# Kernel optimization log

Measured on AMD Instinct MI355X. Metric: run time of the kernel, lower is better.

## Reference

```python
import jax, jax.numpy as jnp
import numpy as np

CACHE_LEN = 1024
EPS = 1e-5

def layer_norm(x, g, b):
    m = jnp.mean(x, axis=-1, keepdims=True)
    var = jnp.mean(jnp.square(x - m), axis=-1, keepdims=True)
    return (x - m) * jax.lax.rsqrt(var + EPS) * g + b

def setup_inputs() -> dict:
    key = jax.random.key(0)
    ks = jax.random.split(key, 16)
    B, Lq, Lk, D_IN, D_OUT = 4, 4096, 5119, 512, 512
    s = 1.0 / np.sqrt(D_IN)
    return {
        "q": jax.random.normal(ks[0], (B, Lq, D_IN), jnp.float32),
        "k": jax.random.normal(ks[1], (B, Lk, D_IN), jnp.float32),
        "v": jax.random.normal(ks[2], (B, Lk, D_IN), jnp.float32),
        "gq": jnp.ones((D_IN,), jnp.float32),
        "bq": jnp.zeros((D_IN,), jnp.float32),
        "gk": jnp.ones((D_IN,), jnp.float32),
        "bk": jnp.zeros((D_IN,), jnp.float32),
        "gv": jnp.ones((D_IN,), jnp.float32),
        "bv": jnp.zeros((D_IN,), jnp.float32),
        "Wq": jax.random.uniform(ks[3], (D_IN, D_OUT), jnp.float32, -s, s),
        "bwq": jax.random.uniform(ks[4], (D_OUT,), jnp.float32, -s, s),
        "Wk": jax.random.uniform(ks[5], (D_IN, D_OUT), jnp.float32, -s, s),
        "bwk": jax.random.uniform(ks[6], (D_OUT,), jnp.float32, -s, s),
        "Wv": jax.random.uniform(ks[7], (D_IN, D_OUT), jnp.float32, -s, s),
        "bwv": jax.random.uniform(ks[8], (D_OUT,), jnp.float32, -s, s),
    }

def reference(q, k, v, gq, bq, gk, bk, gv, bv, Wq, bwq, Wk, bwk, Wv, bwv):
    B, Lq, _ = q.shape
    Lk = k.shape[1]
    qp = layer_norm(q, gq, bq) @ Wq + bwq            # [B,Lq,Do]
    kp = layer_norm(k, gk, bk) @ Wk + bwk            # [B,Lk,Do]
    vp = layer_norm(v, gv, bv) @ Wv + bwv            # [B,Lk,Do]
    kv = jax.nn.relu(kp) * vp                         # [B,Lk,Do]
    # integrate3 skew-pad builds a banded ones mask: query row i attends to
    # kv columns [sup+i, sup+i+cache_len-1]. Equivalent sliding-window sum
    # computed via prefix sums (O(Lk*d) instead of O(Lq*Lk*d)).
    sup = Lk - Lq - CACHE_LEN + 1
    cs = jnp.cumsum(kv, axis=1)
    cs = jnp.concatenate([jnp.zeros_like(cs[:, :1]), cs], axis=1)  # [B,Lk+1,Do]
    starts = sup + jnp.arange(Lq)
    weighted = cs[:, starts + CACHE_LEN] - cs[:, starts]            # [B,Lq,Do]
    return jax.nn.relu(qp) * weighted
```

## Files before the change

kernel.cpp:

```cpp
#include <hip/hip_runtime.h>

#define B     4
#define LQ    4096
#define LK    5119
#define D     512
#define CACHE 1024
#define MQ    (B * LQ)
#define MK    (B * LK)
#define MKP   20480
#define NCH   160
#define TI    32

typedef float  f32x4  __attribute__((ext_vector_type(4)));
typedef __bf16 bf16x2 __attribute__((ext_vector_type(2)));
typedef __bf16 bf16x4 __attribute__((ext_vector_type(4)));
typedef __bf16 bf16x8 __attribute__((ext_vector_type(8)));

__device__ __forceinline__ void async16(void* lds, const void* g)
{
    __builtin_amdgcn_global_load_lds(
        (__attribute__((address_space(1))) void*)(g),
        (__attribute__((address_space(3))) void*)(lds),
        16, 0, 0);
}

__global__ __launch_bounds__(64) void ln_kernel(
    const float* __restrict__ q, const float* __restrict__ k,
    const float* __restrict__ v,
    const float* __restrict__ gq, const float* __restrict__ bq,
    const float* __restrict__ gk, const float* __restrict__ bk,
    const float* __restrict__ gv, const float* __restrict__ bv,
    __bf16* __restrict__ qn, __bf16* __restrict__ kn, __bf16* __restrict__ vn)
{
    const int z = blockIdx.y;
    const float *x, *g, *bb; __bf16* o; int M;
    if (z == 0)      { x = q; g = gq; bb = bq; o = qn; M = MQ; }
    else if (z == 1) { x = k; g = gk; bb = bk; o = kn; M = MK; }
    else             { x = v; g = gv; bb = bv; o = vn; M = MK; }
    const int r = blockIdx.x;
    if (r >= M) return;

    const int t = threadIdx.x;
    const float* xr = x + (long)r * D;
    const float4 a0 = *reinterpret_cast<const float4*>(xr + t * 4);
    const float4 a1 = *reinterpret_cast<const float4*>(xr + 256 + t * 4);

    float s  = a0.x + a0.y + a0.z + a0.w + a1.x + a1.y + a1.z + a1.w;
    float ss = a0.x*a0.x + a0.y*a0.y + a0.z*a0.z + a0.w*a0.w
             + a1.x*a1.x + a1.y*a1.y + a1.z*a1.z + a1.w*a1.w;
#pragma unroll
    for (int m = 1; m < 64; m <<= 1) {
        s  += __shfl_xor(s,  m, 64);
        ss += __shfl_xor(ss, m, 64);
    }
    const float mean = s * (1.f / (float)D);
    const float var  = ss * (1.f / (float)D) - mean * mean;
    const float rs   = rsqrtf(var + 1e-5f);

    const float4 g0 = *reinterpret_cast<const float4*>(g + t * 4);
    const float4 g1 = *reinterpret_cast<const float4*>(g + 256 + t * 4);
    const float4 b0 = *reinterpret_cast<const float4*>(bb + t * 4);
    const float4 b1 = *reinterpret_cast<const float4*>(bb + 256 + t * 4);

    bf16x4 o0, o1;
    o0[0] = (__bf16)((a0.x - mean) * rs * g0.x + b0.x);
    o0[1] = (__bf16)((a0.y - mean) * rs * g0.y + b0.y);
    o0[2] = (__bf16)((a0.z - mean) * rs * g0.z + b0.z);
    o0[3] = (__bf16)((a0.w - mean) * rs * g0.w + b0.w);
    o1[0] = (__bf16)((a1.x - mean) * rs * g1.x + b1.x);
    o1[1] = (__bf16)((a1.y - mean) * rs * g1.y + b1.y);
    o1[2] = (__bf16)((a1.z - mean) * rs * g1.z + b1.z);
    o1[3] = (__bf16)((a1.w - mean) * rs * g1.w + b1.w);

    __bf16* orow = o + (long)r * D;
    *reinterpret_cast<bf16x4*>(orow + t * 4)       = o0;
    *reinterpret_cast<bf16x4*>(orow + 256 + t * 4) = o1;
}

__global__ __launch_bounds__(256) void wconv_kernel(
    const float* __restrict__ Wq, const float* __restrict__ Wk,
    const float* __restrict__ Wv,
    __bf16* __restrict__ wtq, __bf16* __restrict__ wtk, __bf16* __restrict__ wtv)
{
    const int z = blockIdx.z;
    const float* W = (z == 0) ? Wq : (z == 1) ? Wk : Wv;
    __bf16*     Wt = (z == 0) ? wtq : (z == 1) ? wtk : wtv;
    const int n  = blockIdx.x * 256 + threadIdx.x;
    const int k0 = blockIdx.y * 8;
    bf16x8 o;
#pragma unroll
    for (int j = 0; j < 8; ++j)
        o[j] = (__bf16)W[(long)(k0 + j) * D + n];
    *reinterpret_cast<bf16x8*>(Wt + (long)n * D + k0) = o;
}

__global__ __launch_bounds__(256) void gemm_q_kernel(
    const __bf16* __restrict__ A, const __bf16* __restrict__ Wt,
    const float* __restrict__ bias, __bf16* __restrict__ Cout)
{
    __shared__ __attribute__((aligned(16))) __bf16 As[128 * 32];
    __shared__ __attribute__((aligned(16))) __bf16 Bs[128 * 32];

    const int tid  = threadIdx.x;
    const int lane = tid & 63;
    const int wave = tid >> 6;
    const int quad = lane >> 4;
    const int l16  = lane & 15;
    const int wm   = wave >> 1;
    const int wn   = wave & 1;

    f32x4 acc[4][4];
#pragma unroll
    for (int i = 0; i < 4; ++i)
#pragma unroll
        for (int j = 0; j < 4; ++j)
            acc[i][j] = (f32x4){0.f, 0.f, 0.f, 0.f};

    const long arow0 = (long)blockIdx.x * 128;
    const long brow0 = (long)blockIdx.y * 128;
    const int  srow  = lane >> 2;
    const int  scol  = (lane & 3) * 8;

    for (int k0 = 0; k0 < D; k0 += 32) {
#pragma unroll
        for (int h = 0; h < 2; ++h) {
            const int chunk = h * 4 + wave;
            const int row   = chunk * 16 + srow;
            async16(&As[chunk * 512], &A [(arow0 + row) * D + k0 + scol]);
            async16(&Bs[chunk * 512], &Wt[(brow0 + row) * D + k0 + scol]);
        }
        __syncthreads();

        bf16x8 af[4], bfr[4];
#pragma unroll
        for (int tm = 0; tm < 4; ++tm)
            af[tm] = *reinterpret_cast<const bf16x8*>(
                &As[(wm * 64 + tm * 16 + l16) * 32 + quad * 8]);
#pragma unroll
        for (int tn = 0; tn < 4; ++tn)
            bfr[tn] = *reinterpret_cast<const bf16x8*>(
                &Bs[(wn * 64 + tn * 16 + l16) * 32 + quad * 8]);

#pragma unroll
        for (int tm = 0; tm < 4; ++tm)
#pragma unroll
            for (int tn = 0; tn < 4; ++tn)
                acc[tm][tn] = __builtin_amdgcn_mfma_f32_16x16x32_bf16(
                    af[tm], bfr[tn], acc[tm][tn], 0, 0, 0);
        __syncthreads();
    }

#pragma unroll
    for (int tm = 0; tm < 4; ++tm) {
        const long row0 = arow0 + wm * 64 + tm * 16 + quad * 4;
#pragma unroll
        for (int tn = 0; tn < 4; ++tn) {
            const int col = (int)brow0 + wn * 64 + tn * 16 + l16;
            const float bv = bias[col];
#pragma unroll
            for (int r = 0; r < 4; ++r)
                Cout[(row0 + r) * D + col] =
                    (__bf16)fmaxf(acc[tm][tn][r] + bv, 0.f);
        }
    }
}

__global__ __launch_bounds__(256) void gemm_kv_kernel(
    const __bf16* __restrict__ Ak, const __bf16* __restrict__ Av,
    const __bf16* __restrict__ Wtk, const __bf16* __restrict__ Wtv,
    const float* __restrict__ bk, const float* __restrict__ bv,
    __bf16* __restrict__ kvout)
{
    __shared__ __attribute__((aligned(16))) __bf16 Ks [128 * 32];
    __shared__ __attribute__((aligned(16))) __bf16 Vs [128 * 32];
    __shared__ __attribute__((aligned(16))) __bf16 WKs[128 * 32];
    __shared__ __attribute__((aligned(16))) __bf16 WVs[128 * 32];

    const int tid  = threadIdx.x;
    const int lane = tid & 63;
    const int wave = tid >> 6;
    const int quad = lane >> 4;
    const int l16  = lane & 15;
    const int wm   = wave >> 1;
    const int wn   = wave & 1;

    f32x4 acck[4][4], accv[4][4];
#pragma unroll
    for (int i = 0; i < 4; ++i)
#pragma unroll
        for (int j = 0; j < 4; ++j) {
            acck[i][j] = (f32x4){0.f, 0.f, 0.f, 0.f};
            accv[i][j] = (f32x4){0.f, 0.f, 0.f, 0.f};
        }

    const long arow0 = (long)blockIdx.x * 128;
    const long brow0 = (long)blockIdx.y * 128;
    const int  srow  = lane >> 2;
    const int  scol  = (lane & 3) * 8;

    for (int k0 = 0; k0 < D; k0 += 32) {
#pragma unroll
        for (int h = 0; h < 2; ++h) {
            const int chunk = h * 4 + wave;
            const int row   = chunk * 16 + srow;
            async16(&Ks [chunk * 512], &Ak [(arow0 + row) * D + k0 + scol]);
            async16(&Vs [chunk * 512], &Av [(arow0 + row) * D + k0 + scol]);
            async16(&WKs[chunk * 512], &Wtk[(brow0 + row) * D + k0 + scol]);
            async16(&WVs[chunk * 512], &Wtv[(brow0 + row) * D + k0 + scol]);
        }
        __syncthreads();

        bf16x8 fa[4], fb[4];
#pragma unroll
        for (int tm = 0; tm < 4; ++tm)
            fa[tm] = *reinterpret_cast<const bf16x8*>(
                &Ks[(wm * 64 + tm * 16 + l16) * 32 + quad * 8]);
#pragma unroll
        for (int tn = 0; tn < 4; ++tn)
            fb[tn] = *reinterpret_cast<const bf16x8*>(
                &WKs[(wn * 64 + tn * 16 + l16) * 32 + quad * 8]);
#pragma unroll
        for (int tm = 0; tm < 4; ++tm)
#pragma unroll
            for (int tn = 0; tn < 4; ++tn)
                acck[tm][tn] = __builtin_amdgcn_mfma_f32_16x16x32_bf16(
                    fa[tm], fb[tn], acck[tm][tn], 0, 0, 0);

#pragma unroll
        for (int tm = 0; tm < 4; ++tm)
            fa[tm] = *reinterpret_cast<const bf16x8*>(
                &Vs[(wm * 64 + tm * 16 + l16) * 32 + quad * 8]);
#pragma unroll
        for (int tn = 0; tn < 4; ++tn)
            fb[tn] = *reinterpret_cast<const bf16x8*>(
                &WVs[(wn * 64 + tn * 16 + l16) * 32 + quad * 8]);
#pragma unroll
        for (int tm = 0; tm < 4; ++tm)
#pragma unroll
            for (int tn = 0; tn < 4; ++tn)
                accv[tm][tn] = __builtin_amdgcn_mfma_f32_16x16x32_bf16(
                    fa[tm], fb[tn], accv[tm][tn], 0, 0, 0);
        __syncthreads();
    }

#pragma unroll
    for (int tm = 0; tm < 4; ++tm) {
        const long row0 = arow0 + wm * 64 + tm * 16 + quad * 4;
#pragma unroll
        for (int tn = 0; tn < 4; ++tn) {
            const int col = (int)brow0 + wn * 64 + tn * 16 + l16;
            const float bkc = bk[col];
            const float bvc = bv[col];
#pragma unroll
            for (int r = 0; r < 4; ++r) {
                const float kp = fmaxf(acck[tm][tn][r] + bkc, 0.f);
                const float vp = accv[tm][tn][r] + bvc;
                kvout[(row0 + r) * D + col] = (__bf16)(kp * vp);
            }
        }
    }
}

__global__ __launch_bounds__(256) void chunk_kernel(
    const __bf16* __restrict__ kv, float* __restrict__ Csum)
{
    const int c    = blockIdx.x;
    const int b    = blockIdx.y;
    const int col2 = threadIdx.x * 2;
    const __bf16* base = kv + ((long)b * LK + (long)c * 32) * D + col2;
    float s0 = 0.f, s1 = 0.f;
#pragma unroll
    for (int j = 0; j < 32; ++j) {
        const bf16x2 vv = *reinterpret_cast<const bf16x2*>(base + (long)j * D);
        s0 += (float)vv[0];
        s1 += (float)vv[1];
    }
    float* o = Csum + ((long)b * NCH + c) * D + col2;
    o[0] = s0; o[1] = s1;
}

__global__ __launch_bounds__(256) void window_kernel(
    const __bf16* __restrict__ kv, const float* __restrict__ Csum,
    const __bf16* __restrict__ qpb, float* __restrict__ out)
{
    const int iq   = blockIdx.x;
    const int b    = blockIdx.y;
    const int i0   = iq * TI;
    const int col2 = threadIdx.x * 2;

    const float* cs = Csum + (long)b * NCH * D + col2;
    float s0 = 0.f, s1 = 0.f;
#pragma unroll
    for (int c = 0; c < 32; ++c) {
        const float2 cv = *reinterpret_cast<const float2*>(cs + (long)(iq + c) * D);
        s0 += cv.x; s1 += cv.y;
    }

    const __bf16* kvb = kv  + (long)b * LK * D + col2;
    const __bf16* qb  = qpb + (long)b * LQ * D + col2;
    float*        ob  = out + (long)b * LQ * D + col2;

#pragma unroll 8
    for (int i = i0; i < i0 + TI; ++i) {
        const bf16x2 qv = *reinterpret_cast<const bf16x2*>(qb + (long)i * D);
        *reinterpret_cast<float2*>(ob + (long)i * D) =
            make_float2((float)qv[0] * s0, (float)qv[1] * s1);
        const bf16x2 lead  = *reinterpret_cast<const bf16x2*>(kvb + (long)(i + CACHE) * D);
        const bf16x2 trail = *reinterpret_cast<const bf16x2*>(kvb + (long)i * D);
        s0 += (float)lead[0] - (float)trail[0];
        s1 += (float)lead[1] - (float)trail[1];
    }
}

extern "C" void kernel_launch(void* const* d_in, const int* in_sizes, int n_in,
                              void* d_out, int out_size, void* d_ws, size_t ws_size,
                              hipStream_t stream)
{
    const float* q   = (const float*)d_in[0];
    const float* k   = (const float*)d_in[1];
    const float* v   = (const float*)d_in[2];
    const float* gq  = (const float*)d_in[3];
    const float* bq  = (const float*)d_in[4];
    const float* gk  = (const float*)d_in[5];
    const float* bk  = (const float*)d_in[6];
    const float* gv  = (const float*)d_in[7];
    const float* bv  = (const float*)d_in[8];
    const float* Wq  = (const float*)d_in[9];
    const float* bwq = (const float*)d_in[10];
    const float* Wk  = (const float*)d_in[11];
    const float* bwk = (const float*)d_in[12];
    const float* Wv  = (const float*)d_in[13];
    const float* bwv = (const float*)d_in[14];
    float* out = (float*)d_out;

    char* ws = (char*)d_ws;
    __bf16* qn   = (__bf16*)ws;
    __bf16* kn   = qn  + (long)MQ  * D;
    __bf16* vn   = kn  + (long)MKP * D;
    __bf16* qpb  = vn  + (long)MKP * D;
    __bf16* kvb  = qpb + (long)MQ  * D;
    __bf16* wtq  = kvb + (long)MKP * D;
    __bf16* wtk  = wtq + (long)D * D;
    __bf16* wtv  = wtk + (long)D * D;
    float*  Csum = (float*)(wtv + (long)D * D);

    ln_kernel<<<dim3(MK, 3), 64, 0, stream>>>(q, k, v, gq, bq, gk, bk, gv, bv,
                                              qn, kn, vn);
    wconv_kernel<<<dim3(2, 64, 3), 256, 0, stream>>>(Wq, Wk, Wv, wtq, wtk, wtv);

    gemm_q_kernel<<<dim3(MQ / 128, D / 128), 256, 0, stream>>>(qn, wtq, bwq, qpb);

    gemm_kv_kernel<<<dim3(MKP / 128, D / 128), 256, 0, stream>>>(
        kn, vn, wtk, wtv, bwk, bwv, kvb);

    chunk_kernel<<<dim3(NCH, B), 256, 0, stream>>>(kvb, Csum);

    window_kernel<<<dim3(LQ / TI, B), 256, 0, stream>>>(kvb, Csum, qpb, out);
}
```

Baseline: 273.0 us.

## Shrink GEMM N-tile to 64, swizzle LDS layout, and batch four LN rows per block

The Q and KV GEMMs now use 128x64 output tiles instead of 128x128. This doubles the grid, halves the accumulator registers, and lets launch bounds request two blocks per CU. Staging into shared memory now uses an XOR swizzle on the 16-byte column chunks, with matching swizzled fragment reads, to cut LDS bank conflicts. The layernorm kernel packs four rows per 256-thread block, so it launches a quarter as many blocks. The trade-off is less reuse of the A tile per block and more reloading of A across N tiles.

```diff
diff --git a/kernel.cpp b/kernel.cpp
--- a/kernel.cpp
+++ b/kernel.cpp
@@ -24,7 +24,7 @@
         16, 0, 0);
 }
 
-__global__ __launch_bounds__(64) void ln_kernel(
+__global__ __launch_bounds__(256) void ln_kernel(
     const float* __restrict__ q, const float* __restrict__ k,
     const float* __restrict__ v,
     const float* __restrict__ gq, const float* __restrict__ bq,
@@ -37,10 +37,10 @@
     if (z == 0)      { x = q; g = gq; bb = bq; o = qn; M = MQ; }
     else if (z == 1) { x = k; g = gk; bb = bk; o = kn; M = MK; }
     else             { x = v; g = gv; bb = bv; o = vn; M = MK; }
-    const int r = blockIdx.x;
+    const int r = blockIdx.x * 4 + (threadIdx.x >> 6);
     if (r >= M) return;
 
-    const int t = threadIdx.x;
+    const int t = threadIdx.x & 63;
     const float* xr = x + (long)r * D;
     const float4 a0 = *reinterpret_cast<const float4*>(xr + t * 4);
     const float4 a1 = *reinterpret_cast<const float4*>(xr + 256 + t * 4);
@@ -94,12 +94,12 @@
     *reinterpret_cast<bf16x8*>(Wt + (long)n * D + k0) = o;
 }
 
-__global__ __launch_bounds__(256) void gemm_q_kernel(
+__global__ __launch_bounds__(256, 2) void gemm_q_kernel(
     const __bf16* __restrict__ A, const __bf16* __restrict__ Wt,
     const float* __restrict__ bias, __bf16* __restrict__ Cout)
 {
     __shared__ __attribute__((aligned(16))) __bf16 As[128 * 32];
-    __shared__ __attribute__((aligned(16))) __bf16 Bs[128 * 32];
+    __shared__ __attribute__((aligned(16))) __bf16 Bs[64 * 32];
 
     const int tid  = threadIdx.x;
     const int lane = tid & 63;
@@ -109,42 +109,42 @@
     const int wm   = wave >> 1;
     const int wn   = wave & 1;
 
-    f32x4 acc[4][4];
+    f32x4 acc[4][2];
 #pragma unroll
     for (int i = 0; i < 4; ++i)
 #pragma unroll
-        for (int j = 0; j < 4; ++j)
+        for (int j = 0; j < 2; ++j)
             acc[i][j] = (f32x4){0.f, 0.f, 0.f, 0.f};
 
     const long arow0 = (long)blockIdx.x * 128;
-    const long brow0 = (long)blockIdx.y * 128;
+    const long brow0 = (long)blockIdx.y * 64;
     const int  srow  = lane >> 2;
-    const int  scol  = (lane & 3) * 8;
+    const int  scol  = (((lane & 3) ^ ((srow >> 1) & 3)) * 8);
+    const int  soff  = ((quad ^ ((l16 >> 1) & 3)) * 8);
 
     for (int k0 = 0; k0 < D; k0 += 32) {
-#pragma unroll
-        for (int h = 0; h < 2; ++h) {
-            const int chunk = h * 4 + wave;
-            const int row   = chunk * 16 + srow;
-            async16(&As[chunk * 512], &A [(arow0 + row) * D + k0 + scol]);
-            async16(&Bs[chunk * 512], &Wt[(brow0 + row) * D + k0 + scol]);
-        }
+        async16(&As[wave * 512],
+                &A[(arow0 + wave * 16 + srow) * D + k0 + scol]);
+        async16(&As[(wave + 4) * 512],
+                &A[(arow0 + (wave + 4) * 16 + srow) * D + k0 + scol]);
+        async16(&Bs[wave * 512],
+                &Wt[(brow0 + wave * 16 + srow) * D + k0 + scol]);
         __syncthreads();
 
-        bf16x8 af[4], bfr[4];
+        bf16x8 af[4], bfr[2];
 #pragma unroll
         for (int tm = 0; tm < 4; ++tm)
             af[tm] = *reinterpret_cast<const bf16x8*>(
-                &As[(wm * 64 + tm * 16 + l16) * 32 + quad * 8]);
-#pragma unroll
-        for (int tn = 0; tn < 4; ++tn)
+                &As[(wm * 64 + tm * 16 + l16) * 32 + soff]);
+#pragma unroll
+        for (int tn = 0; tn < 2; ++tn)
             bfr[tn] = *reinterpret_cast<const bf16x8*>(
-                &Bs[(wn * 64 + tn * 16 + l16) * 32 + quad * 8]);
-
-#pragma unroll
-        for (int tm = 0; tm < 4; ++tm)
-#pragma unroll
-            for (int tn = 0; tn < 4; ++tn)
+                &Bs[(wn * 32 + tn * 16 + l16) * 32 + soff]);
+
+#pragma unroll
+        for (int tm = 0; tm < 4; ++tm)
+#pragma unroll
+            for (int tn = 0; tn < 2; ++tn)
                 acc[tm][tn] = __builtin_amdgcn_mfma_f32_16x16x32_bf16(
                     af[tm], bfr[tn], acc[tm][tn], 0, 0, 0);
         __syncthreads();
@@ -154,8 +154,8 @@
     for (int tm = 0; tm < 4; ++tm) {
         const long row0 = arow0 + wm * 64 + tm * 16 + quad * 4;
 #pragma unroll
-        for (int tn = 0; tn < 4; ++tn) {
-            const int col = (int)brow0 + wn * 64 + tn * 16 + l16;
+        for (int tn = 0; tn < 2; ++tn) {
+            const int col = (int)brow0 + wn * 32 + tn * 16 + l16;
             const float bv = bias[col];
 #pragma unroll
             for (int r = 0; r < 4; ++r)
@@ -165,7 +165,7 @@
     }
 }
 
-__global__ __launch_bounds__(256) void gemm_kv_kernel(
+__global__ __launch_bounds__(256, 2) void gemm_kv_kernel(
     const __bf16* __restrict__ Ak, const __bf16* __restrict__ Av,
     const __bf16* __restrict__ Wtk, const __bf16* __restrict__ Wtv,
     const float* __restrict__ bk, const float* __restrict__ bv,
@@ -173,8 +173,8 @@
 {
     __shared__ __attribute__((aligned(16))) __bf16 Ks [128 * 32];
     __shared__ __attribute__((aligned(16))) __bf16 Vs [128 * 32];
-    __shared__ __attribute__((aligned(16))) __bf16 WKs[128 * 32];
-    __shared__ __attribute__((aligned(16))) __bf16 WVs[128 * 32];
+    __shared__ __attribute__((aligned(16))) __bf16 WKs[64 * 32];
+    __shared__ __attribute__((aligned(16))) __bf16 WVs[64 * 32];
 
     const int tid  = threadIdx.x;
     const int lane = tid & 63;
@@ -184,60 +184,64 @@
     const int wm   = wave >> 1;
     const int wn   = wave & 1;
 
-    f32x4 acck[4][4], accv[4][4];
+    f32x4 acck[4][2], accv[4][2];
 #pragma unroll
     for (int i = 0; i < 4; ++i)
 #pragma unroll
-        for (int j = 0; j < 4; ++j) {
+        for (int j = 0; j < 2; ++j) {
             acck[i][j] = (f32x4){0.f, 0.f, 0.f, 0.f};
             accv[i][j] = (f32x4){0.f, 0.f, 0.f, 0.f};
         }
 
     const long arow0 = (long)blockIdx.x * 128;
-    const long brow0 = (long)blockIdx.y * 128;
+    const long brow0 = (long)blockIdx.y * 64;
     const int  srow  = lane >> 2;
-    const int  scol  = (lane & 3) * 8;
+    const int  scol  = (((lane & 3) ^ ((srow >> 1) & 3)) * 8);
+    const int  soff  = ((quad ^ ((l16 >> 1) & 3)) * 8);
 
     for (int k0 = 0; k0 < D; k0 += 32) {
-#pragma unroll
-        for (int h = 0; h < 2; ++h) {
-            const int chunk = h * 4 + wave;
-            const int row   = chunk * 16 + srow;
-            async16(&Ks [chunk * 512], &Ak [(arow0 + row) * D + k0 + scol]);
-            async16(&Vs [chunk * 512], &Av [(arow0 + row) * D + k0 + scol]);
-            async16(&WKs[chunk * 512], &Wtk[(brow0 + row) * D + k0 + scol]);
-            async16(&WVs[chunk * 512], &Wtv[(brow0 + row) * D + k0 + scol]);
-        }
+        async16(&Ks[wave * 512],
+                &Ak[(arow0 + wave * 16 + srow) * D + k0 + scol]);
+        async16(&Ks[(wave + 4) * 512],
+                &Ak[(arow0 + (wave + 4) * 16 + srow) * D + k0 + scol]);
+        async16(&Vs[wave * 512],
+                &Av[(arow0 + wave * 16 + srow) * D + k0 + scol]);
+        async16(&Vs[(wave + 4) * 512],
+                &Av[(arow0 + (wave + 4) * 16 + srow) * D + k0 + scol]);
+        async16(&WKs[wave * 512],
+                &Wtk[(brow0 + wave * 16 + srow) * D + k0 + scol]);
+        async16(&WVs[wave * 512],
+                &Wtv[(brow0 + wave * 16 + srow) * D + k0 + scol]);
         __syncthreads();
 
-        bf16x8 fa[4], fb[4];
+        bf16x8 fa[4], fb[2];
 #pragma unroll
         for (int tm = 0; tm < 4; ++tm)
             fa[tm] = *reinterpret_cast<const bf16x8*>(
-                &Ks[(wm * 64 + tm * 16 + l16) * 32 + quad * 8]);
-#pragma unroll
-        for (int tn = 0; tn < 4; ++tn)
+                &Ks[(wm * 64 + tm * 16 + l16) * 32 + soff]);
+#pragma unroll
+        for (int tn = 0; tn < 2; ++tn)
             fb[tn] = *reinterpret_cast<const bf16x8*>(
-                &WKs[(wn * 64 + tn * 16 + l16) * 32 + quad * 8]);
-#pragma unroll
-        for (int tm = 0; tm < 4; ++tm)
-#pragma unroll
-            for (int tn = 0; tn < 4; ++tn)
+                &WKs[(wn * 32 + tn * 16 + l16) * 32 + soff]);
+#pragma unroll
+        for (int tm = 0; tm < 4; ++tm)
+#pragma unroll
+            for (int tn = 0; tn < 2; ++tn)
                 acck[tm][tn] = __builtin_amdgcn_mfma_f32_16x16x32_bf16(
                     fa[tm], fb[tn], acck[tm][tn], 0, 0, 0);
 
 #pragma unroll
         for (int tm = 0; tm < 4; ++tm)
             fa[tm] = *reinterpret_cast<const bf16x8*>(
-                &Vs[(wm * 64 + tm * 16 + l16) * 32 + quad * 8]);
-#pragma unroll
-        for (int tn = 0; tn < 4; ++tn)
+                &Vs[(wm * 64 + tm * 16 + l16) * 32 + soff]);
+#pragma unroll
+        for (int tn = 0; tn < 2; ++tn)
             fb[tn] = *reinterpret_cast<const bf16x8*>(
-                &WVs[(wn * 64 + tn * 16 + l16) * 32 + quad * 8]);
-#pragma unroll
-        for (int tm = 0; tm < 4; ++tm)
-#pragma unroll
-            for (int tn = 0; tn < 4; ++tn)
+                &WVs[(wn * 32 + tn * 16 + l16) * 32 + soff]);
+#pragma unroll
+        for (int tm = 0; tm < 4; ++tm)
+#pragma unroll
+            for (int tn = 0; tn < 2; ++tn)
                 accv[tm][tn] = __builtin_amdgcn_mfma_f32_16x16x32_bf16(
                     fa[tm], fb[tn], accv[tm][tn], 0, 0, 0);
         __syncthreads();
@@ -247,8 +251,8 @@
     for (int tm = 0; tm < 4; ++tm) {
         const long row0 = arow0 + wm * 64 + tm * 16 + quad * 4;
 #pragma unroll
-        for (int tn = 0; tn < 4; ++tn) {
-            const int col = (int)brow0 + wn * 64 + tn * 16 + l16;
+        for (int tn = 0; tn < 2; ++tn) {
+            const int col = (int)brow0 + wn * 32 + tn * 16 + l16;
             const float bkc = bk[col];
             const float bvc = bv[col];
 #pragma unroll
@@ -344,13 +348,13 @@
     __bf16* wtv  = wtk + (long)D * D;
     float*  Csum = (float*)(wtv + (long)D * D);
 
-    ln_kernel<<<dim3(MK, 3), 64, 0, stream>>>(q, k, v, gq, bq, gk, bk, gv, bv,
-                                              qn, kn, vn);
+    ln_kernel<<<dim3(5120, 3), 256, 0, stream>>>(q, k, v, gq, bq, gk, bk, gv, bv,
+                                                 qn, kn, vn);
     wconv_kernel<<<dim3(2, 64, 3), 256, 0, stream>>>(Wq, Wk, Wv, wtq, wtk, wtv);
 
-    gemm_q_kernel<<<dim3(MQ / 128, D / 128), 256, 0, stream>>>(qn, wtq, bwq, qpb);
-
-    gemm_kv_kernel<<<dim3(MKP / 128, D / 128), 256, 0, stream>>>(
+    gemm_q_kernel<<<dim3(MQ / 128, D / 64), 256, 0, stream>>>(qn, wtq, bwq, qpb);
+
+    gemm_kv_kernel<<<dim3(MKP / 128, D / 64), 256, 0, stream>>>(
         kn, vn, wtk, wtv, bwk, bwv, kvb);
 
     chunk_kernel<<<dim3(NCH, B), 256, 0, stream>>>(kvb, Csum);
```

Measured after the change: 252.0 us. 7.7% less time.
